# Kernel optimization log

Measured on AMD Instinct MI355X. Metric: run time of the kernel, lower is better.

The kernel has to match this reference:

```python
import jax, jax.numpy as jnp
import numpy as np

D_MODEL = 512
N_HEADS = 8
DH = D_MODEL // N_HEADS


def _split_heads(x, h):
    B, L, D = x.shape
    return x.reshape(B, L, h, D // h).transpose(0, 2, 1, 3)  # [B,h,L,Dh]


def setup_inputs() -> dict:
    key = jax.random.key(0)
    ks = jax.random.split(key, 10)
    B, La, Lb, Lc = 4, 256, 256, 32
    s = 1.0 / np.sqrt(D_MODEL)
    return {
        "Q_in": jax.random.normal(ks[0], (B, La, D_MODEL), jnp.float32),
        "K_in": jax.random.normal(ks[1], (B, Lb, D_MODEL), jnp.float32),
        "V_in": jax.random.normal(ks[2], (B, Lb, D_MODEL), jnp.float32),
        "C_tokens": jax.random.normal(ks[3], (B, Lc, D_MODEL), jnp.float32),
        "Wq": jax.random.normal(ks[4], (D_MODEL, D_MODEL), jnp.float32) * s,
        "bq": jnp.zeros((D_MODEL,), jnp.float32),
        "Wk": jax.random.normal(ks[5], (D_MODEL, D_MODEL), jnp.float32) * s,
        "bk": jnp.zeros((D_MODEL,), jnp.float32),
        "Wv": jax.random.normal(ks[6], (D_MODEL, D_MODEL), jnp.float32) * s,
        "bv": jnp.zeros((D_MODEL,), jnp.float32),
    }


def reference(Q_in, K_in, V_in, C_tokens, Wq, bq, Wk, bk, Wv, bv):
    B, La, D = Q_in.shape
    Lb = K_in.shape[1]
    Lc = C_tokens.shape[1]
    h = N_HEADS
    # torch Linear: y = x @ W.T + b
    Q = _split_heads(Q_in @ Wq.T + bq, h)        # [B,h,La,Dh]
    K = _split_heads(K_in @ Wk.T + bk, h)        # [B,h,Lb,Dh]
    V = _split_heads(V_in @ Wv.T + bv, h)        # [B,h,Lb,Dh]
    C = _split_heads(C_tokens, h)                # [B,h,Lc,Dh]
    # tri-linear TSDP score: [B,h,La,Lb,Lc]
    scores = jnp.einsum('bhqd,bhkd,bhcd->bhqkc', Q, K, C) / np.sqrt(DH)
    scores = scores.reshape(B, h, La, Lb * Lc)
    attn = jax.nn.softmax(scores, axis=-1)       # no mask path; all_masked trivially False
    attn5 = attn.reshape(B, h, La, Lb, Lc)
    # cv_mode='mul': VC[k,c,d] = V[k,d]*C[c,d]; fuse contraction, never materialize VC
    out = jnp.einsum('bhqkc,bhkd,bhcd->bhqd', attn5, V, C)
    out = out.transpose(0, 2, 1, 3).reshape(B, La, D)
    return (out, attn)
```

## Files before the change

### kernel.cpp

```cpp
#include <hip/hip_runtime.h>
#include <hip/hip_bf16.h>
#include <math.h>

#define D_MODEL 512
#define NH 8
#define DH 64
#define LA 256
#define LB 256
#define LC 32
#define BATCH 4
#define KC_TOT 8192
#define XN (BATCH * LA * D_MODEL)
#define WN (D_MODEL * D_MODEL)

typedef float f32x4 __attribute__((ext_vector_type(4)));
typedef _Float16 f16x8 __attribute__((ext_vector_type(8)));
typedef _Float16 f16x4 __attribute__((ext_vector_type(4)));
typedef unsigned int u32;

#if __has_builtin(__builtin_amdgcn_exp2f)
#define EXP2(x) __builtin_amdgcn_exp2f(x)
#else
#define EXP2(x) exp2f(x)
#endif
#define SCLOG2E 0.18033688011118324f

#define MFMA16F(a, b, c) __builtin_amdgcn_mfma_f32_16x16x32_f16(a, b, c, 0, 0, 0)

static __device__ __forceinline__ u32 pkrtz(float x, float y) {
  auto t = __builtin_amdgcn_cvt_pkrtz(x, y);
  u32 r; __builtin_memcpy(&r, &t, 4);
  return r;
}

__global__ __launch_bounds__(256) void cvt_kernel(
    const float* __restrict__ X0, const float* __restrict__ X1,
    const float* __restrict__ X2, const float* __restrict__ W0,
    const float* __restrict__ W1, const float* __restrict__ W2,
    _Float16* __restrict__ dst)
{
  const int t = blockIdx.y;
  const float* src;
  size_t n, off;
  switch (t) {
    case 0: src = X0; n = XN; off = 0; break;
    case 1: src = X1; n = XN; off = (size_t)XN; break;
    case 2: src = X2; n = XN; off = 2 * (size_t)XN; break;
    case 3: src = W0; n = WN; off = 3 * (size_t)XN; break;
    case 4: src = W1; n = WN; off = 3 * (size_t)XN + WN; break;
    default: src = W2; n = WN; off = 3 * (size_t)XN + 2 * (size_t)WN; break;
  }
  const size_t i = (size_t)blockIdx.x * 2048 + threadIdx.x * 8;
  if (i >= n) return;
  float4 a = *(const float4*)(src + i);
  float4 b = *(const float4*)(src + i + 4);
  f16x8 r;
  r[0] = (_Float16)a.x; r[1] = (_Float16)a.y; r[2] = (_Float16)a.z; r[3] = (_Float16)a.w;
  r[4] = (_Float16)b.x; r[5] = (_Float16)b.y; r[6] = (_Float16)b.z; r[7] = (_Float16)b.w;
  *(f16x8*)(dst + off + i) = r;
}

__global__ __launch_bounds__(256) void proj_mfma(
    const _Float16* __restrict__ XWh,
    const float* __restrict__ bq, const float* __restrict__ bk,
    const float* __restrict__ bv,
    _Float16* __restrict__ Qp, _Float16* __restrict__ Kp,
    _Float16* __restrict__ Vp)
{
  const int z = blockIdx.z;
  const _Float16* X = XWh + (size_t)z * XN;
  const _Float16* W = XWh + 3 * (size_t)XN + (size_t)z * WN;
  const float* bias = (z == 0) ? bq : (z == 1) ? bk : bv;
  _Float16* Y = (z == 0) ? Qp : (z == 1) ? Kp : Vp;

  const int tid = threadIdx.x;
  const int lane = tid & 63;
  const int w = tid >> 6;
  const int l16 = lane & 15;
  const int lg = lane >> 4;

  const int n0 = blockIdx.x * 64;
  const int m0 = blockIdx.y * 64;
  const int m = m0 + w * 16 + l16;

  f32x4 acc[4] = {};
  const _Float16* xrow = X + (size_t)m * D_MODEL;
  const _Float16* wbase = W + (size_t)(n0 + l16) * D_MODEL;

#pragma unroll 4
  for (int ks = 0; ks < 16; ++ks) {
    f16x8 bf = *(const f16x8*)(xrow + ks * 32 + lg * 8);
#pragma unroll
    for (int ai = 0; ai < 4; ++ai) {
      f16x8 af = *(const f16x8*)(wbase + (size_t)(ai * 16) * D_MODEL + ks * 32 + lg * 8);
      acc[ai] = MFMA16F(af, bf, acc[ai]);
    }
  }
#pragma unroll
  for (int ai = 0; ai < 4; ++ai) {
    float4 b4 = *(const float4*)&bias[n0 + ai * 16 + lg * 4];
    f16x4 r;
    r[0] = (_Float16)(acc[ai][0] + b4.x);
    r[1] = (_Float16)(acc[ai][1] + b4.y);
    r[2] = (_Float16)(acc[ai][2] + b4.z);
    r[3] = (_Float16)(acc[ai][3] + b4.w);
    *(f16x4*)&Y[(size_t)m * D_MODEL + n0 + ai * 16 + lg * 4] = r;
  }
}

__global__ __launch_bounds__(512) void attn_fused(
    const _Float16* __restrict__ Qp, const _Float16* __restrict__ Kp,
    const _Float16* __restrict__ Vp, const float* __restrict__ Ct,
    float* __restrict__ attn, float* __restrict__ out)
{
  __shared__ __align__(16) _Float16 K_lds[LB][DH];
  __shared__ __align__(16) _Float16 C_lds[LC][DH + 8];
  __shared__ __align__(16) _Float16 CT_lds[DH][LC + 8];
  __shared__ float red_lds[8][16];
  __shared__ float inv_lds[16];

  const int tid = threadIdx.x;
  const int lane = tid & 63;
  const int w = tid >> 6;
  const int l16 = lane & 15;
  const int lg = lane >> 4;

  const int tile = blockIdx.x;
  const int bh = tile >> 4;
  const int qt = tile & 15;
  const int b = bh >> 3;
  const int h = bh & 7;

  const _Float16* Kb = Kp + (size_t)b * LB * D_MODEL + h * DH;
  const _Float16* Vb = Vp + (size_t)b * LB * D_MODEL + h * DH;
  const float* Cb = Ct + (size_t)b * LC * D_MODEL + h * DH;

  for (int i = tid; i < LB * DH / 8; i += 512) {
    const int k = i >> 3, dg = (i & 7) * 8;
    *(f16x8*)&K_lds[k][dg] = *(const f16x8*)(Kb + (size_t)k * D_MODEL + dg);
  }
  for (int i = tid; i < LC * DH; i += 512) {
    const int c = i >> 6, d = i & 63;
    _Float16 v = (_Float16)Cb[(size_t)c * D_MODEL + d];
    C_lds[c][d] = v;
    CT_lds[d][c] = v;
  }

  f16x8 qf[2];
  {
    const _Float16* Qb = Qp + (size_t)(b * LA + qt * 16) * D_MODEL + h * DH;
#pragma unroll
    for (int kh = 0; kh < 2; ++kh)
      qf[kh] = *(const f16x8*)(Qb + (size_t)l16 * D_MODEL + kh * 32 + lg * 8);
  }
  __syncthreads();

  float rs = 0.f;
#pragma unroll 2
  for (int ch = 0; ch < 32; ++ch) {
    const int krow = w * 32 + ch;
    f32x4 s0 = {0.f, 0.f, 0.f, 0.f}, s1 = {0.f, 0.f, 0.f, 0.f};
#pragma unroll
    for (int kh = 0; kh < 2; ++kh) {
      f16x8 kv = *(const f16x8*)&K_lds[krow][kh * 32 + lg * 8];
      f16x8 c0 = *(const f16x8*)&C_lds[l16][kh * 32 + lg * 8];
      f16x8 c1 = *(const f16x8*)&C_lds[16 + l16][kh * 32 + lg * 8];
      s0 = MFMA16F(kv * c0, qf[kh], s0);
      s1 = MFMA16F(kv * c1, qf[kh], s1);
    }
#pragma unroll
    for (int r = 0; r < 4; ++r)
      rs += EXP2(s0[r] * SCLOG2E) + EXP2(s1[r] * SCLOG2E);
  }
  rs += __shfl_xor(rs, 16);
  rs += __shfl_xor(rs, 32);
  if (lane < 16) red_lds[w][lane] = rs;
  __syncthreads();
  if (tid < 16) {
    float t = 0.f;
#pragma unroll
    for (int ww = 0; ww < 8; ++ww) t += red_lds[ww][tid];
    inv_lds[tid] = 1.f / t;
  }
  __syncthreads();
  const float inv = inv_lds[l16];

  f32x4 oacc[4] = {};
  float* arow = attn + (size_t)(bh * LA + qt * 16 + l16) * KC_TOT + w * 1024;
  const int s1i = l16 + ((lg & 1) << 5);
  const int s2i = s1i + 16;

#pragma unroll 2
  for (int ch = 0; ch < 32; ++ch) {
    const int krow = w * 32 + ch;
    f32x4 s0 = {0.f, 0.f, 0.f, 0.f}, s1 = {0.f, 0.f, 0.f, 0.f};
#pragma unroll
    for (int kh = 0; kh < 2; ++kh) {
      f16x8 kv = *(const f16x8*)&K_lds[krow][kh * 32 + lg * 8];
      f16x8 c0 = *(const f16x8*)&C_lds[l16][kh * 32 + lg * 8];
      f16x8 c1 = *(const f16x8*)&C_lds[16 + l16][kh * 32 + lg * 8];
      s0 = MFMA16F(kv * c0, qf[kh], s0);
      s1 = MFMA16F(kv * c1, qf[kh], s1);
    }
    f32x4 p0, p1;
#pragma unroll
    for (int r = 0; r < 4; ++r) {
      p0[r] = EXP2(s0[r] * SCLOG2E) * inv;
      p1[r] = EXP2(s1[r] * SCLOG2E) * inv;
    }
    *(f32x4*)(arow + ch * 32 + lg * 4) = p0;
    *(f32x4*)(arow + ch * 32 + 16 + lg * 4) = p1;

    const u32 a0 = pkrtz(p0[0], p0[1]), a1 = pkrtz(p0[2], p0[3]);
    const u32 b0 = pkrtz(p1[0], p1[1]), b1 = pkrtz(p1[2], p1[3]);
    const u32 sa0 = (u32)__shfl((int)a0, s1i), sb0 = (u32)__shfl((int)b0, s1i);
    const u32 sa1 = (u32)__shfl((int)a1, s1i), sb1 = (u32)__shfl((int)b1, s1i);
    const u32 ta0 = (u32)__shfl((int)a0, s2i), tb0 = (u32)__shfl((int)b0, s2i);
    const u32 ta1 = (u32)__shfl((int)a1, s2i), tb1 = (u32)__shfl((int)b1, s2i);
    u32 bw[4];
    bw[0] = (lg < 2) ? sa0 : sb0;
    bw[1] = (lg < 2) ? sa1 : sb1;
    bw[2] = (lg < 2) ? ta0 : tb0;
    bw[3] = (lg < 2) ? ta1 : tb1;
    f16x8 bf; __builtin_memcpy(&bf, bw, 16);

    const _Float16* vrow = Vb + (size_t)krow * D_MODEL;
#pragma unroll
    for (int dt = 0; dt < 4; ++dt) {
      const _Float16 vv = vrow[dt * 16 + l16];
      f16x8 ct8 = *(const f16x8*)&CT_lds[dt * 16 + l16][lg * 8];
      oacc[dt] = MFMA16F(ct8 * vv, bf, oacc[dt]);
    }
  }

  __syncthreads();
  float* obuf = (float*)&K_lds[0][0];
#pragma unroll
  for (int dt = 0; dt < 4; ++dt)
#pragma unroll
    for (int r = 0; r < 4; ++r)
      obuf[w * 1024 + l16 * 64 + dt * 16 + lg * 4 + r] = oacc[dt][r];
  __syncthreads();
  for (int e = tid; e < 1024; e += 512) {
    float t = 0.f;
#pragma unroll
    for (int ww = 0; ww < 8; ++ww) t += obuf[ww * 1024 + e];
    const int qq = e >> 6, d = e & 63;
    out[(size_t)(b * LA + qt * 16 + qq) * D_MODEL + h * DH + d] = t;
  }
}

extern "C" void kernel_launch(void* const* d_in, const int* in_sizes, int n_in,
                              void* d_out, int out_size, void* d_ws, size_t ws_size,
                              hipStream_t stream) {
  const float* Q_in     = (const float*)d_in[0];
  const float* K_in     = (const float*)d_in[1];
  const float* V_in     = (const float*)d_in[2];
  const float* C_tokens = (const float*)d_in[3];
  const float* Wq       = (const float*)d_in[4];
  const float* bq       = (const float*)d_in[5];
  const float* Wk       = (const float*)d_in[6];
  const float* bk       = (const float*)d_in[7];
  const float* Wv       = (const float*)d_in[8];
  const float* bv       = (const float*)d_in[9];

  float* outp  = (float*)d_out;
  float* attnp = outp + (size_t)BATCH * LA * D_MODEL;

  _Float16* Qp  = (_Float16*)d_ws;
  _Float16* Kp  = Qp + (size_t)XN;
  _Float16* Vp  = Kp + (size_t)XN;
  _Float16* XWh = Vp + (size_t)XN;

  cvt_kernel<<<dim3(256, 6), 256, 0, stream>>>(Q_in, K_in, V_in, Wq, Wk, Wv, XWh);
  proj_mfma<<<dim3(8, 16, 3), 256, 0, stream>>>(XWh, bq, bk, bv, Qp, Kp, Vp);
  attn_fused<<<512, 512, 0, stream>>>(Qp, Kp, Vp, C_tokens, attnp, outp);
}
```

Baseline: 103.4 us.

## Stage attention-probability stores through LDS and read K directly from global

Each wave now writes its softmax probabilities into a small double-buffered LDS tile. One iteration later it reads the tile back with a lane mapping that gives 128-byte contiguous row segments per store instead of 64-byte fragments, aiming to coalesce the large attn output writes better. The K LDS preload is removed and K rows are loaded straight from global or cache inside the score loops, which frees LDS for the staging buffer. The cost is extra LDS traffic per chunk and possibly higher K load latency, since K is now read twice from cache rather than from LDS.

Result: faster. 92.98 us (-10.0%).

```diff
diff --git a/kernel.cpp b/kernel.cpp
--- a/kernel.cpp
+++ b/kernel.cpp
@@ -108,12 +108,13 @@
   }
 }
 
+#define STG 40
 __global__ __launch_bounds__(512) void attn_fused(
     const _Float16* __restrict__ Qp, const _Float16* __restrict__ Kp,
     const _Float16* __restrict__ Vp, const float* __restrict__ Ct,
     float* __restrict__ attn, float* __restrict__ out)
 {
-  __shared__ __align__(16) _Float16 K_lds[LB][DH];
+  __shared__ __align__(16) float stage[8][2][16][STG];
   __shared__ __align__(16) _Float16 C_lds[LC][DH + 8];
   __shared__ __align__(16) _Float16 CT_lds[DH][LC + 8];
   __shared__ float red_lds[8][16];
@@ -135,10 +136,6 @@
   const _Float16* Vb = Vp + (size_t)b * LB * D_MODEL + h * DH;
   const float* Cb = Ct + (size_t)b * LC * D_MODEL + h * DH;
 
-  for (int i = tid; i < LB * DH / 8; i += 512) {
-    const int k = i >> 3, dg = (i & 7) * 8;
-    *(f16x8*)&K_lds[k][dg] = *(const f16x8*)(Kb + (size_t)k * D_MODEL + dg);
-  }
   for (int i = tid; i < LC * DH; i += 512) {
     const int c = i >> 6, d = i & 63;
     _Float16 v = (_Float16)Cb[(size_t)c * D_MODEL + d];
@@ -159,10 +156,11 @@
 #pragma unroll 2
   for (int ch = 0; ch < 32; ++ch) {
     const int krow = w * 32 + ch;
+    const _Float16* krp = Kb + (size_t)krow * D_MODEL;
     f32x4 s0 = {0.f, 0.f, 0.f, 0.f}, s1 = {0.f, 0.f, 0.f, 0.f};
 #pragma unroll
     for (int kh = 0; kh < 2; ++kh) {
-      f16x8 kv = *(const f16x8*)&K_lds[krow][kh * 32 + lg * 8];
+      f16x8 kv = *(const f16x8*)(krp + kh * 32 + lg * 8);
       f16x8 c0 = *(const f16x8*)&C_lds[l16][kh * 32 + lg * 8];
       f16x8 c1 = *(const f16x8*)&C_lds[16 + l16][kh * 32 + lg * 8];
       s0 = MFMA16F(kv * c0, qf[kh], s0);
@@ -186,17 +184,21 @@
   const float inv = inv_lds[l16];
 
   f32x4 oacc[4] = {};
-  float* arow = attn + (size_t)(bh * LA + qt * 16 + l16) * KC_TOT + w * 1024;
   const int s1i = l16 + ((lg & 1) << 5);
   const int s2i = s1i + 16;
+  const int strow = lane >> 3;
+  const int stcol = (lane & 7) * 4;
+  float* abase = attn + (size_t)(bh * LA + qt * 16) * KC_TOT + w * 1024;
 
 #pragma unroll 2
   for (int ch = 0; ch < 32; ++ch) {
     const int krow = w * 32 + ch;
+    const int cur = ch & 1;
+    const _Float16* krp = Kb + (size_t)krow * D_MODEL;
     f32x4 s0 = {0.f, 0.f, 0.f, 0.f}, s1 = {0.f, 0.f, 0.f, 0.f};
 #pragma unroll
     for (int kh = 0; kh < 2; ++kh) {
-      f16x8 kv = *(const f16x8*)&K_lds[krow][kh * 32 + lg * 8];
+      f16x8 kv = *(const f16x8*)(krp + kh * 32 + lg * 8);
       f16x8 c0 = *(const f16x8*)&C_lds[l16][kh * 32 + lg * 8];
       f16x8 c1 = *(const f16x8*)&C_lds[16 + l16][kh * 32 + lg * 8];
       s0 = MFMA16F(kv * c0, qf[kh], s0);
@@ -208,8 +210,8 @@
       p0[r] = EXP2(s0[r] * SCLOG2E) * inv;
       p1[r] = EXP2(s1[r] * SCLOG2E) * inv;
     }
-    *(f32x4*)(arow + ch * 32 + lg * 4) = p0;
-    *(f32x4*)(arow + ch * 32 + 16 + lg * 4) = p1;
+    *(f32x4*)&stage[w][cur][l16][lg * 4] = p0;
+    *(f32x4*)&stage[w][cur][l16][16 + lg * 4] = p1;
 
     const u32 a0 = pkrtz(p0[0], p0[1]), a1 = pkrtz(p0[2], p0[3]);
     const u32 b0 = pkrtz(p1[0], p1[1]), b1 = pkrtz(p1[2], p1[3]);
@@ -231,10 +233,25 @@
       f16x8 ct8 = *(const f16x8*)&CT_lds[dt * 16 + l16][lg * 8];
       oacc[dt] = MFMA16F(ct8 * vv, bf, oacc[dt]);
     }
-  }
-
-  __syncthreads();
-  float* obuf = (float*)&K_lds[0][0];
+
+    if (ch > 0) {
+      const int pc = ch - 1;
+      const int pb = pc & 1;
+      f32x4 v0 = *(const f32x4*)&stage[w][pb][strow][stcol];
+      f32x4 v1 = *(const f32x4*)&stage[w][pb][strow + 8][stcol];
+      *(f32x4*)(abase + (size_t)strow * KC_TOT + pc * 32 + stcol) = v0;
+      *(f32x4*)(abase + (size_t)(strow + 8) * KC_TOT + pc * 32 + stcol) = v1;
+    }
+  }
+  {
+    f32x4 v0 = *(const f32x4*)&stage[w][1][strow][stcol];
+    f32x4 v1 = *(const f32x4*)&stage[w][1][strow + 8][stcol];
+    *(f32x4*)(abase + (size_t)strow * KC_TOT + 31 * 32 + stcol) = v0;
+    *(f32x4*)(abase + (size_t)(strow + 8) * KC_TOT + 31 * 32 + stcol) = v1;
+  }
+
+  __syncthreads();
+  float* obuf = &stage[0][0][0][0];
 #pragma unroll
   for (int dt = 0; dt < 4; ++dt)
 #pragma unroll
```

## Stage attn tiles in LDS for coalesced stores and read K from global

Applied to the files above, without the earlier changes.

The softmax probabilities are written into a per-wave LDS staging buffer covering four k-rows, then copied out as contiguous 512-byte row segments per half-wave. Before, each lane stored scattered 16-byte pieces into rows far apart. The shared K tile is removed and K rows are read straight from global/L1 in both passes, which frees LDS for the staging buffer. The cost is extra LDS write/read traffic and repeated global K loads with no block sync around the stage, which is safe because each wave only touches its own slice.

Measured after the change: 107.6 us. 1.04x slower.

```diff
diff --git a/kernel.cpp b/kernel.cpp
--- a/kernel.cpp
+++ b/kernel.cpp
@@ -108,12 +108,13 @@
   }
 }
 
+#define STG 132
 __global__ __launch_bounds__(512) void attn_fused(
     const _Float16* __restrict__ Qp, const _Float16* __restrict__ Kp,
     const _Float16* __restrict__ Vp, const float* __restrict__ Ct,
     float* __restrict__ attn, float* __restrict__ out)
 {
-  __shared__ __align__(16) _Float16 K_lds[LB][DH];
+  __shared__ __align__(16) float stage[8][16][STG];
   __shared__ __align__(16) _Float16 C_lds[LC][DH + 8];
   __shared__ __align__(16) _Float16 CT_lds[DH][LC + 8];
   __shared__ float red_lds[8][16];
@@ -135,10 +136,6 @@
   const _Float16* Vb = Vp + (size_t)b * LB * D_MODEL + h * DH;
   const float* Cb = Ct + (size_t)b * LC * D_MODEL + h * DH;
 
-  for (int i = tid; i < LB * DH / 8; i += 512) {
-    const int k = i >> 3, dg = (i & 7) * 8;
-    *(f16x8*)&K_lds[k][dg] = *(const f16x8*)(Kb + (size_t)k * D_MODEL + dg);
-  }
   for (int i = tid; i < LC * DH; i += 512) {
     const int c = i >> 6, d = i & 63;
     _Float16 v = (_Float16)Cb[(size_t)c * D_MODEL + d];
@@ -159,10 +156,11 @@
 #pragma unroll 2
   for (int ch = 0; ch < 32; ++ch) {
     const int krow = w * 32 + ch;
+    const _Float16* krp = Kb + (size_t)krow * D_MODEL;
     f32x4 s0 = {0.f, 0.f, 0.f, 0.f}, s1 = {0.f, 0.f, 0.f, 0.f};
 #pragma unroll
     for (int kh = 0; kh < 2; ++kh) {
-      f16x8 kv = *(const f16x8*)&K_lds[krow][kh * 32 + lg * 8];
+      f16x8 kv = *(const f16x8*)(krp + kh * 32 + lg * 8);
       f16x8 c0 = *(const f16x8*)&C_lds[l16][kh * 32 + lg * 8];
       f16x8 c1 = *(const f16x8*)&C_lds[16 + l16][kh * 32 + lg * 8];
       s0 = MFMA16F(kv * c0, qf[kh], s0);
@@ -186,55 +184,69 @@
   const float inv = inv_lds[l16];
 
   f32x4 oacc[4] = {};
-  float* arow = attn + (size_t)(bh * LA + qt * 16 + l16) * KC_TOT + w * 1024;
   const int s1i = l16 + ((lg & 1) << 5);
   const int s2i = s1i + 16;
-
-#pragma unroll 2
-  for (int ch = 0; ch < 32; ++ch) {
-    const int krow = w * 32 + ch;
-    f32x4 s0 = {0.f, 0.f, 0.f, 0.f}, s1 = {0.f, 0.f, 0.f, 0.f};
-#pragma unroll
-    for (int kh = 0; kh < 2; ++kh) {
-      f16x8 kv = *(const f16x8*)&K_lds[krow][kh * 32 + lg * 8];
-      f16x8 c0 = *(const f16x8*)&C_lds[l16][kh * 32 + lg * 8];
-      f16x8 c1 = *(const f16x8*)&C_lds[16 + l16][kh * 32 + lg * 8];
-      s0 = MFMA16F(kv * c0, qf[kh], s0);
-      s1 = MFMA16F(kv * c1, qf[kh], s1);
-    }
-    f32x4 p0, p1;
-#pragma unroll
-    for (int r = 0; r < 4; ++r) {
-      p0[r] = EXP2(s0[r] * SCLOG2E) * inv;
-      p1[r] = EXP2(s1[r] * SCLOG2E) * inv;
-    }
-    *(f32x4*)(arow + ch * 32 + lg * 4) = p0;
-    *(f32x4*)(arow + ch * 32 + 16 + lg * 4) = p1;
-
-    const u32 a0 = pkrtz(p0[0], p0[1]), a1 = pkrtz(p0[2], p0[3]);
-    const u32 b0 = pkrtz(p1[0], p1[1]), b1 = pkrtz(p1[2], p1[3]);
-    const u32 sa0 = (u32)__shfl((int)a0, s1i), sb0 = (u32)__shfl((int)b0, s1i);
-    const u32 sa1 = (u32)__shfl((int)a1, s1i), sb1 = (u32)__shfl((int)b1, s1i);
-    const u32 ta0 = (u32)__shfl((int)a0, s2i), tb0 = (u32)__shfl((int)b0, s2i);
-    const u32 ta1 = (u32)__shfl((int)a1, s2i), tb1 = (u32)__shfl((int)b1, s2i);
-    u32 bw[4];
-    bw[0] = (lg < 2) ? sa0 : sb0;
-    bw[1] = (lg < 2) ? sa1 : sb1;
-    bw[2] = (lg < 2) ? ta0 : tb0;
-    bw[3] = (lg < 2) ? ta1 : tb1;
-    f16x8 bf; __builtin_memcpy(&bf, bw, 16);
-
-    const _Float16* vrow = Vb + (size_t)krow * D_MODEL;
-#pragma unroll
-    for (int dt = 0; dt < 4; ++dt) {
-      const _Float16 vv = vrow[dt * 16 + l16];
-      f16x8 ct8 = *(const f16x8*)&CT_lds[dt * 16 + l16][lg * 8];
-      oacc[dt] = MFMA16F(ct8 * vv, bf, oacc[dt]);
-    }
-  }
-
-  __syncthreads();
-  float* obuf = (float*)&K_lds[0][0];
+  const int strow = lane >> 5;
+  const int stcol = (lane & 31) * 4;
+  float* abase = attn + (size_t)(bh * LA + qt * 16) * KC_TOT + w * 1024;
+
+#pragma unroll 1
+  for (int g = 0; g < 8; ++g) {
+#pragma unroll
+    for (int cc = 0; cc < 4; ++cc) {
+      const int ch = g * 4 + cc;
+      const int krow = w * 32 + ch;
+      const _Float16* krp = Kb + (size_t)krow * D_MODEL;
+      f32x4 s0 = {0.f, 0.f, 0.f, 0.f}, s1 = {0.f, 0.f, 0.f, 0.f};
+#pragma unroll
+      for (int kh = 0; kh < 2; ++kh) {
+        f16x8 kv = *(const f16x8*)(krp + kh * 32 + lg * 8);
+        f16x8 c0 = *(const f16x8*)&C_lds[l16][kh * 32 + lg * 8];
+        f16x8 c1 = *(const f16x8*)&C_lds[16 + l16][kh * 32 + lg * 8];
+        s0 = MFMA16F(kv * c0, qf[kh], s0);
+        s1 = MFMA16F(kv * c1, qf[kh], s1);
+      }
+      f32x4 p0, p1;
+#pragma unroll
+      for (int r = 0; r < 4; ++r) {
+        p0[r] = EXP2(s0[r] * SCLOG2E) * inv;
+        p1[r] = EXP2(s1[r] * SCLOG2E) * inv;
+      }
+      *(f32x4*)&stage[w][l16][cc * 32 + lg * 4] = p0;
+      *(f32x4*)&stage[w][l16][cc * 32 + 16 + lg * 4] = p1;
+
+      const u32 a0 = pkrtz(p0[0], p0[1]), a1 = pkrtz(p0[2], p0[3]);
+      const u32 b0 = pkrtz(p1[0], p1[1]), b1 = pkrtz(p1[2], p1[3]);
+      const u32 sa0 = (u32)__shfl((int)a0, s1i), sb0 = (u32)__shfl((int)b0, s1i);
+      const u32 sa1 = (u32)__shfl((int)a1, s1i), sb1 = (u32)__shfl((int)b1, s1i);
+      const u32 ta0 = (u32)__shfl((int)a0, s2i), tb0 = (u32)__shfl((int)b0, s2i);
+      const u32 ta1 = (u32)__shfl((int)a1, s2i), tb1 = (u32)__shfl((int)b1, s2i);
+      u32 bw[4];
+      bw[0] = (lg < 2) ? sa0 : sb0;
+      bw[1] = (lg < 2) ? sa1 : sb1;
+      bw[2] = (lg < 2) ? ta0 : tb0;
+      bw[3] = (lg < 2) ? ta1 : tb1;
+      f16x8 bf; __builtin_memcpy(&bf, bw, 16);
+
+      const _Float16* vrow = Vb + (size_t)krow * D_MODEL;
+#pragma unroll
+      for (int dt = 0; dt < 4; ++dt) {
+        const _Float16 vv = vrow[dt * 16 + l16];
+        f16x8 ct8 = *(const f16x8*)&CT_lds[dt * 16 + l16][lg * 8];
+        oacc[dt] = MFMA16F(ct8 * vv, bf, oacc[dt]);
+      }
+    }
+
+#pragma unroll
+    for (int i = 0; i < 8; ++i) {
+      const int row = i * 2 + strow;
+      f32x4 v = *(const f32x4*)&stage[w][row][stcol];
+      *(f32x4*)(abase + (size_t)row * KC_TOT + g * 128 + stcol) = v;
+    }
+  }
+
+  __syncthreads();
+  float* obuf = &stage[0][0][0];
 #pragma unroll
   for (int dt = 0; dt < 4; ++dt)
 #pragma unroll
```
